# Performance work log

Hardware: AMD Instinct MI355X
Metric: run time of the kernel (lower is better)

## Reference

```python
import jax, jax.numpy as jnp
import numpy as np

N, E, R, D = 100000, 1600000, 8, 128

def setup_inputs() -> dict:
    key = jax.random.key(0)
    ks = jax.random.split(key, 8)
    x = jax.random.normal(ks[0], (N, D), dtype=jnp.float32)
    src = jax.random.randint(ks[1], (E,), 0, N, dtype=jnp.int32)
    dst = jax.random.randint(ks[2], (E,), 0, N, dtype=jnp.int32)
    etype = jax.random.randint(ks[3], (E,), 0, R, dtype=jnp.int32)
    W_rel = jax.random.normal(ks[4], (R, D, D), dtype=jnp.float32) * 0.05
    loop_w = jax.random.normal(ks[5], (D, D), dtype=jnp.float32) * 0.05
    rel_bias = jnp.zeros((D,), dtype=jnp.float32)
    W1 = jax.random.normal(ks[6], (2 * D, 2 * D), dtype=jnp.float32) * 0.05
    b1 = jnp.zeros((2 * D,), dtype=jnp.float32)
    W2 = jax.random.normal(ks[7], (3 * D, D), dtype=jnp.float32) * 0.05
    b2 = jnp.zeros((D,), dtype=jnp.float32)
    return {"x": x, "src": src, "dst": dst, "etype": etype,
            "W_rel": W_rel, "loop_w": loop_w, "rel_bias": rel_bias,
            "W1": W1, "b1": b1, "W2": W2, "b2": b2}

def reference(x, src, dst, etype, W_rel, loop_w, rel_bias, W1, b1, W2, b2):
    # RelGraphConv (low_mem): aggregate source features per (relation, dst) node,
    # then one matmul per relation: msg[i] = sum_r (sum_{e: etype=r, dst=i} x[src_e]) @ W_r
    seg = etype.astype(jnp.int32) * N + dst.astype(jnp.int32)  # combined (rel, dst) id
    agg = jax.ops.segment_sum(x[src], seg, num_segments=R * N)  # [R*N, D]
    agg = agg.reshape(R, N, D)
    msg = jnp.einsum('rnd,rdo->no', agg, W_rel)  # per-relation transform + sum over relations
    msg = msg + x @ loop_w + rel_bias            # DGL default self_loop + bias
    # concat-MLP update (activation = tanh)
    mid = jnp.tanh(jnp.concatenate([x, msg], axis=1) @ W1 + b1)  # [N, 2D]
    out = jnp.concatenate([x, mid], axis=1) @ W2 + b2            # [N, D]
    return out
```

## Files before the change

### kernel.cpp

```cpp
#include <hip/hip_runtime.h>

#define NN 100000
#define DD 128
#define RR 8
#define NSEG (RR*NN)
#define NB1 782
#define ECAP 2048

typedef unsigned short u16;
typedef __bf16 bf16x8 __attribute__((ext_vector_type(8)));
typedef float f32x4 __attribute__((ext_vector_type(4)));
typedef u16 ushort4e __attribute__((ext_vector_type(4)));
typedef unsigned int uint4e __attribute__((ext_vector_type(4)));

__device__ __forceinline__ u16 f2bf(float f){
    union { float f; unsigned u; } v; v.f = f;
    unsigned r = v.u + 0x7fffu + ((v.u >> 16) & 1u);
    return (u16)(r >> 16);
}
__device__ __forceinline__ float bf2f(u16 h){
    union { unsigned u; float f; } v; v.u = ((unsigned)h) << 16; return v.f;
}
__device__ __forceinline__ float ftanh(float x){
    float e = __expf(2.0f * x);
    return 1.0f - 2.0f / (e + 1.0f);
}
__device__ __forceinline__ bf16x8 ldv(const u16* p){
    return *reinterpret_cast<const bf16x8*>(p);
}
__device__ __forceinline__ void gload_lds16(const void* g, void* l){
    __builtin_amdgcn_global_load_lds(
        (const __attribute__((address_space(1))) void*)g,
        (__attribute__((address_space(3))) void*)l, 16, 0, 0);
}

__global__ void k_prep1(const float* __restrict__ x, u16* __restrict__ xb,
                        const float* __restrict__ Wrel, const float* __restrict__ loopw,
                        const float* __restrict__ W1, const float* __restrict__ W2,
                        u16* __restrict__ WT, u16* __restrict__ W1t, u16* __restrict__ W2t,
                        const int* __restrict__ et, const int* __restrict__ dst,
                        int* __restrict__ cnt, int* __restrict__ seg, int E){
    const int bid = blockIdx.x;
    if (bid < 12500){
        int i = (bid * 256 + threadIdx.x) * 4;
        float4 v = *reinterpret_cast<const float4*>(x + i);
        ushort4 o = make_ushort4(f2bf(v.x), f2bf(v.y), f2bf(v.z), f2bf(v.w));
        *reinterpret_cast<ushort4*>(xb + i) = o;
    } else if (bid < 13524){
        int tid = (bid - 12500) * 256 + threadIdx.x;
        if (tid < 131072) {
            int r = tid >> 14, rem = tid & 16383, d = rem >> 7, o = rem & 127;
            WT[(r * 128 + o) * 128 + d] = f2bf(Wrel[tid]);
        } else if (tid < 147456) {
            int i = tid - 131072, d = i >> 7, o = i & 127;
            WT[(8 * 128 + o) * 128 + d] = f2bf(loopw[i]);
        } else if (tid < 212992) {
            int i = tid - 147456, k = i >> 8, n2 = i & 255;
            W1t[n2 * 256 + k] = f2bf(W1[i]);
        } else {
            int i = tid - 212992, k = i >> 7, n2 = i & 127;
            W2t[n2 * 384 + k] = f2bf(W2[i]);
        }
    } else {
        int e = (bid - 13524) * 256 + threadIdx.x;
        if (e < E){
            int s = et[e] * NN + dst[e];
            seg[e] = s;
            atomicAdd(&cnt[s], 1);
        }
    }
}

__global__ void k_scan1(const int* __restrict__ cnt, int* __restrict__ Off, int* __restrict__ bsum){
    __shared__ int lds[256];
    int t = threadIdx.x;
    int i0 = blockIdx.x * 1024 + t * 4;
    int c0 = (i0 + 0 < NSEG) ? cnt[i0 + 0] : 0;
    int c1 = (i0 + 1 < NSEG) ? cnt[i0 + 1] : 0;
    int c2 = (i0 + 2 < NSEG) ? cnt[i0 + 2] : 0;
    int c3 = (i0 + 3 < NSEG) ? cnt[i0 + 3] : 0;
    int s = c0 + c1 + c2 + c3;
    lds[t] = s; __syncthreads();
    for (int off = 1; off < 256; off <<= 1){
        int v = (t >= off) ? lds[t - off] : 0;
        __syncthreads();
        lds[t] += v;
        __syncthreads();
    }
    int excl = lds[t] - s;
    if (i0 + 0 < NSEG) Off[i0 + 0] = excl; excl += c0;
    if (i0 + 1 < NSEG) Off[i0 + 1] = excl; excl += c1;
    if (i0 + 2 < NSEG) Off[i0 + 2] = excl; excl += c2;
    if (i0 + 3 < NSEG) Off[i0 + 3] = excl;
    if (t == 255) bsum[blockIdx.x] = s + lds[t] - s;
}

__global__ void k_scan3b(int* __restrict__ Off, const int* __restrict__ bsum,
                         int* __restrict__ cursor, int E){
    __shared__ int lds[256];
    const int bid = blockIdx.x;
    const int t = threadIdx.x;
    int s = 0;
    for (int j = t; j < bid; j += 256) s += bsum[j];
    lds[t] = s; __syncthreads();
    #pragma unroll
    for (int off = 128; off > 0; off >>= 1){
        if (t < off) lds[t] += lds[t + off];
        __syncthreads();
    }
    const int base = lds[0];
    int i0 = bid * 1024 + t * 4;
    #pragma unroll
    for (int j = 0; j < 4; ++j){
        int i = i0 + j;
        if (i < NSEG){ int v = Off[i] + base; Off[i] = v; cursor[i] = v; }
    }
    if (bid == 0 && t == 0) Off[NSEG] = E;
}

__global__ void k_scatter(const int* __restrict__ seg, const int* __restrict__ src,
                          int* __restrict__ cursor, int* __restrict__ esrc, int E){
    int e = blockIdx.x * 256 + threadIdx.x;
    if (e < E){
        int pos = atomicAdd(&cursor[seg[e]], 1);
        esrc[pos] = src[e];
    }
}

__global__ __launch_bounds__(256) void k_agg(
    const u16* __restrict__ xb, const int* __restrict__ Off,
    const int* __restrict__ esrc, u16* __restrict__ agg)
{
    __shared__ int offs[33];
    __shared__ int eidx[ECAP];
    const int tid = threadIdx.x;
    const int s0 = blockIdx.x * 32;
    if (tid < 33) offs[tid] = Off[s0 + tid];
    __syncthreads();
    const int base = offs[0];
    const int tot = offs[32] - base;
    const bool inlds = (tot <= ECAP);
    if (inlds){
        for (int i = tid; i < tot; i += 256) eidx[i] = esrc[base + i];
    }
    __syncthreads();

    const int hw = tid >> 5;
    const int lid = tid & 31;
    const int c = lid * 4;

    #pragma unroll
    for (int j = 0; j < 4; ++j){
        const int sj = hw * 4 + j;
        const int lo = offs[sj] - base;
        const int hi = offs[sj + 1] - base;
        float a0 = 0.f, a1 = 0.f, a2 = 0.f, a3 = 0.f;
        int e = lo;
        if (inlds){
            for (; e + 4 <= hi; e += 4){
                int i0 = eidx[e], i1 = eidx[e+1], i2 = eidx[e+2], i3 = eidx[e+3];
                ushort4 v0 = *reinterpret_cast<const ushort4*>(xb + (size_t)i0 * DD + c);
                ushort4 v1 = *reinterpret_cast<const ushort4*>(xb + (size_t)i1 * DD + c);
                ushort4 v2 = *reinterpret_cast<const ushort4*>(xb + (size_t)i2 * DD + c);
                ushort4 v3 = *reinterpret_cast<const ushort4*>(xb + (size_t)i3 * DD + c);
                a0 += bf2f(v0.x) + bf2f(v1.x) + bf2f(v2.x) + bf2f(v3.x);
                a1 += bf2f(v0.y) + bf2f(v1.y) + bf2f(v2.y) + bf2f(v3.y);
                a2 += bf2f(v0.z) + bf2f(v1.z) + bf2f(v2.z) + bf2f(v3.z);
                a3 += bf2f(v0.w) + bf2f(v1.w) + bf2f(v2.w) + bf2f(v3.w);
            }
            for (; e < hi; ++e){
                int i = eidx[e];
                ushort4 v = *reinterpret_cast<const ushort4*>(xb + (size_t)i * DD + c);
                a0 += bf2f(v.x); a1 += bf2f(v.y); a2 += bf2f(v.z); a3 += bf2f(v.w);
            }
        } else {
            for (; e < hi; ++e){
                int i = esrc[base + e];
                ushort4 v = *reinterpret_cast<const ushort4*>(xb + (size_t)i * DD + c);
                a0 += bf2f(v.x); a1 += bf2f(v.y); a2 += bf2f(v.z); a3 += bf2f(v.w);
            }
        }
        ushort4e o;
        o.x = f2bf(a0); o.y = f2bf(a1); o.z = f2bf(a2); o.w = f2bf(a3);
        __builtin_nontemporal_store(o,
            reinterpret_cast<ushort4e*>(agg + (size_t)(s0 + sj) * DD + c));
    }
}

__global__ __launch_bounds__(512) void k_fused(
    const u16* __restrict__ xb, const u16* __restrict__ agg,
    const u16* __restrict__ WT, const u16* __restrict__ W1t, const u16* __restrict__ W2t,
    const float* __restrict__ relb, const float* __restrict__ bb1, const float* __restrict__ bb2,
    float* __restrict__ out)
{
    __shared__ __align__(16) u16 smem[25088];
    u16 (*bufA)[128] = (u16(*)[128])(smem);
    u16 (*bufB)[128] = (u16(*)[128])(smem + 8192);
    u16 (*msgs)[136] = (u16(*)[136])(smem + 16384);
    u16 (*mids)[264] = (u16(*)[264])(smem + 8192);

    const int tid = threadIdx.x;
    const int w = tid >> 6;
    const int lane = tid & 63;
    const int l15 = lane & 15;
    const int l4 = lane >> 4;
    const int kof = l4 * 8;
    const int swz = (l15 & 7) << 3;
    const int b64 = blockIdx.x * 64;

    const int Wb0 = w * 1024 + (lane << 4);
    auto stage_dma = [&](u16* buf, const u16* grows){
        #pragma unroll
        for (int is = 0; is < 2; ++is){
            int W = Wb0 + is * 8192;
            int row = W >> 8;
            int srcrow = (b64 + row < NN) ? row : 0;
            int inrow = (W & 255) ^ ((row & 7) << 4);
            const char* src = (const char*)(grows + (size_t)srcrow * DD) + inrow;
            gload_lds16(src, (char*)buf + W);
        }
    };

    f32x4 acc[4];
    #pragma unroll
    for (int mi = 0; mi < 4; ++mi)
        #pragma unroll
        for (int q = 0; q < 4; ++q) acc[mi][q] = 0.f;

    stage_dma(&bufA[0][0], agg + (size_t)b64 * DD);
    __syncthreads();

    for (int r = 0; r <= 8; ++r){
        if (r < 7)       stage_dma((r & 1) ? &bufA[0][0] : &bufB[0][0],
                                   agg + ((size_t)(r + 1) * NN + b64) * DD);
        else if (r == 7) stage_dma(&bufA[0][0], xb + (size_t)b64 * DD);
        const u16 (*A)[128] = (r & 1) ? bufB : bufA;
        const u16* B = WT + r * (DD * DD);
        #pragma unroll
        for (int kc = 0; kc < 4; ++kc){
            int cA = (kc * 32 + kof) ^ swz;
            bf16x8 a0 = ldv(&A[l15][cA]);
            bf16x8 a1 = ldv(&A[16 + l15][cA]);
            bf16x8 a2 = ldv(&A[32 + l15][cA]);
            bf16x8 a3 = ldv(&A[48 + l15][cA]);
            bf16x8 wv = ldv(B + (w * 16 + l15) * DD + kc * 32 + kof);
            acc[0] = __builtin_amdgcn_mfma_f32_16x16x32_bf16(a0, wv, acc[0], 0, 0, 0);
            acc[1] = __builtin_amdgcn_mfma_f32_16x16x32_bf16(a1, wv, acc[1], 0, 0, 0);
            acc[2] = __builtin_amdgcn_mfma_f32_16x16x32_bf16(a2, wv, acc[2], 0, 0, 0);
            acc[3] = __builtin_amdgcn_mfma_f32_16x16x32_bf16(a3, wv, acc[3], 0, 0, 0);
        }
        __syncthreads();
    }

    {
        int col = w * 16 + l15;
        float bv = relb[col];
        #pragma unroll
        for (int mi = 0; mi < 4; ++mi)
            #pragma unroll
            for (int q = 0; q < 4; ++q)
                msgs[mi * 16 + l4 * 4 + q][col] = f2bf(acc[mi][q] + bv);
    }
    __syncthreads();

    f32x4 acc2[4][2];
    #pragma unroll
    for (int mi = 0; mi < 4; ++mi)
        #pragma unroll
        for (int nj = 0; nj < 2; ++nj)
            #pragma unroll
            for (int q = 0; q < 4; ++q) acc2[mi][nj][q] = 0.f;

    #pragma unroll
    for (int kc = 0; kc < 8; ++kc){
        bf16x8 a[4];
        #pragma unroll
        for (int mi = 0; mi < 4; ++mi)
            a[mi] = (kc < 4) ? ldv(&bufA[mi * 16 + l15][(kc * 32 + kof) ^ swz])
                             : ldv(&msgs[mi * 16 + l15][(kc - 4) * 32 + kof]);
        #pragma unroll
        for (int nj = 0; nj < 2; ++nj){
            int n2 = w * 32 + nj * 16 + l15;
            bf16x8 wv = ldv(W1t + n2 * 256 + kc * 32 + kof);
            #pragma unroll
            for (int mi = 0; mi < 4; ++mi)
                acc2[mi][nj] = __builtin_amdgcn_mfma_f32_16x16x32_bf16(a[mi], wv, acc2[mi][nj], 0, 0, 0);
        }
    }
    __syncthreads();
    #pragma unroll
    for (int nj = 0; nj < 2; ++nj){
        int col = w * 32 + nj * 16 + l15;
        float bv = bb1[col];
        #pragma unroll
        for (int mi = 0; mi < 4; ++mi)
            #pragma unroll
            for (int q = 0; q < 4; ++q)
                mids[mi * 16 + l4 * 4 + q][col] = f2bf(ftanh(acc2[mi][nj][q] + bv));
    }
    __syncthreads();

    f32x4 acc3[4];
    #pragma unroll
    for (int mi = 0; mi < 4; ++mi)
        #pragma unroll
        for (int q = 0; q < 4; ++q) acc3[mi][q] = 0.f;

    #pragma unroll
    for (int kc = 0; kc < 12; ++kc){
        bf16x8 a[4];
        #pragma unroll
        for (int mi = 0; mi < 4; ++mi)
            a[mi] = (kc < 4) ? ldv(&bufA[mi * 16 + l15][(kc * 32 + kof) ^ swz])
                             : ldv(&mids[mi * 16 + l15][(kc - 4) * 32 + kof]);
        bf16x8 wv = ldv(W2t + (w * 16 + l15) * 384 + kc * 32 + kof);
        #pragma unroll
        for (int mi = 0; mi < 4; ++mi)
            acc3[mi] = __builtin_amdgcn_mfma_f32_16x16x32_bf16(a[mi], wv, acc3[mi], 0, 0, 0);
    }

    {
        int col = w * 16 + l15;
        float bv = bb2[col];
        #pragma unroll
        for (int mi = 0; mi < 4; ++mi)
            #pragma unroll
            for (int q = 0; q < 4; ++q){
                int row = b64 + mi * 16 + l4 * 4 + q;
                if (row < NN)
                    __builtin_nontemporal_store(acc3[mi][q] + bv,
                        &out[(size_t)row * DD + col]);
            }
    }
}

extern "C" void kernel_launch(void* const* d_in, const int* in_sizes, int n_in,
                              void* d_out, int out_size, void* d_ws, size_t ws_size,
                              hipStream_t stream){
    const float* x    = (const float*)d_in[0];
    const int*   src  = (const int*)d_in[1];
    const int*   dst  = (const int*)d_in[2];
    const int*   et   = (const int*)d_in[3];
    const float* Wrel = (const float*)d_in[4];
    const float* loopw= (const float*)d_in[5];
    const float* relb = (const float*)d_in[6];
    const float* W1   = (const float*)d_in[7];
    const float* b1   = (const float*)d_in[8];
    const float* W2   = (const float*)d_in[9];
    const float* b2   = (const float*)d_in[10];
    const int E = in_sizes[1];
    float* out = (float*)d_out;

    char* ws = (char*)d_ws;
    u16* xb   = (u16*)(ws);
    u16* WT   = (u16*)(ws + 25600000);
    u16* W1t  = (u16*)(ws + 25894912);
    u16* W2t  = (u16*)(ws + 26025984);
    int* cnt  = (int*)(ws + 26124288);
    int* Off  = (int*)(ws + 29324288);
    int* bsum = (int*)(ws + 32524544);
    int* esrc = (int*)(ws + 32528640);
    u16* agg  = (u16*)(ws + 38928640);
    int* seg  = (int*)(ws + 38928640);
    if (ws_size < 243728640UL) return;

    const int gprep = 13524 + (E + 255) / 256;
    hipMemsetAsync(cnt, 0, NSEG * sizeof(int), stream);
    k_prep1<<<gprep, 256, 0, stream>>>(x, xb, Wrel, loopw, W1, W2, WT, W1t, W2t,
                                       et, dst, cnt, seg, E);
    k_scan1<<<NB1, 256, 0, stream>>>(cnt, Off, bsum);
    k_scan3b<<<NB1, 256, 0, stream>>>(Off, bsum, cnt, E);
    k_scatter<<<(E + 255) / 256, 256, 0, stream>>>(seg, src, cnt, esrc, E);
    k_agg<<<NSEG / 32, 256, 0, stream>>>(xb, Off, esrc, agg);
    k_fused<<<(NN + 63) / 64, 512, 0, stream>>>(xb, agg, WT, W1t, W2t, relb, b1, b2, out);
}
```

Baseline: 437.0 us.

## Deepen fused-kernel LDS prefetch to four stages with explicit vmcnt waits

```diff
diff --git a/kernel.cpp b/kernel.cpp
--- a/kernel.cpp
+++ b/kernel.cpp
@@ -92,7 +92,7 @@
     if (i0 + 1 < NSEG) Off[i0 + 1] = excl; excl += c1;
     if (i0 + 2 < NSEG) Off[i0 + 2] = excl; excl += c2;
     if (i0 + 3 < NSEG) Off[i0 + 3] = excl;
-    if (t == 255) bsum[blockIdx.x] = s + lds[t] - s;
+    if (t == 255) bsum[blockIdx.x] = lds[255];
 }
 
 __global__ void k_scan3b(int* __restrict__ Off, const int* __restrict__ bsum,
@@ -193,11 +193,10 @@
     const float* __restrict__ relb, const float* __restrict__ bb1, const float* __restrict__ bb2,
     float* __restrict__ out)
 {
-    __shared__ __align__(16) u16 smem[25088];
-    u16 (*bufA)[128] = (u16(*)[128])(smem);
-    u16 (*bufB)[128] = (u16(*)[128])(smem + 8192);
-    u16 (*msgs)[136] = (u16(*)[136])(smem + 16384);
-    u16 (*mids)[264] = (u16(*)[264])(smem + 8192);
+    __shared__ __align__(16) u16 smem[32768];
+    u16* xt   = smem;
+    u16* msgs = smem + 8192;
+    u16* mids = smem + 16384;
 
     const int tid = threadIdx.x;
     const int w = tid >> 6;
@@ -227,29 +226,44 @@
         #pragma unroll
         for (int q = 0; q < 4; ++q) acc[mi][q] = 0.f;
 
-    stage_dma(&bufA[0][0], agg + (size_t)b64 * DD);
-    __syncthreads();
+    #pragma unroll
+    for (int t = 0; t < 4; ++t)
+        stage_dma(smem + t * 8192, agg + ((size_t)t * NN + b64) * DD);
 
     for (int r = 0; r <= 8; ++r){
-        if (r < 7)       stage_dma((r & 1) ? &bufA[0][0] : &bufB[0][0],
-                                   agg + ((size_t)(r + 1) * NN + b64) * DD);
-        else if (r == 7) stage_dma(&bufA[0][0], xb + (size_t)b64 * DD);
-        const u16 (*A)[128] = (r & 1) ? bufB : bufA;
+        __builtin_amdgcn_sched_barrier(0);
+        if (r <= 5)      asm volatile("s_waitcnt vmcnt(6)" ::: "memory");
+        else if (r == 6) asm volatile("s_waitcnt vmcnt(4)" ::: "memory");
+        else if (r == 7) asm volatile("s_waitcnt vmcnt(2)" ::: "memory");
+        else             asm volatile("s_waitcnt vmcnt(0)" ::: "memory");
+        __builtin_amdgcn_sched_barrier(0);
+        __builtin_amdgcn_s_barrier();
+        __builtin_amdgcn_sched_barrier(0);
+
+        const u16* A = smem + (r & 3) * 8192;
         const u16* B = WT + r * (DD * DD);
         #pragma unroll
         for (int kc = 0; kc < 4; ++kc){
             int cA = (kc * 32 + kof) ^ swz;
-            bf16x8 a0 = ldv(&A[l15][cA]);
-            bf16x8 a1 = ldv(&A[16 + l15][cA]);
-            bf16x8 a2 = ldv(&A[32 + l15][cA]);
-            bf16x8 a3 = ldv(&A[48 + l15][cA]);
+            bf16x8 a0 = ldv(A + (l15) * 128 + cA);
+            bf16x8 a1 = ldv(A + (16 + l15) * 128 + cA);
+            bf16x8 a2 = ldv(A + (32 + l15) * 128 + cA);
+            bf16x8 a3 = ldv(A + (48 + l15) * 128 + cA);
             bf16x8 wv = ldv(B + (w * 16 + l15) * DD + kc * 32 + kof);
             acc[0] = __builtin_amdgcn_mfma_f32_16x16x32_bf16(a0, wv, acc[0], 0, 0, 0);
             acc[1] = __builtin_amdgcn_mfma_f32_16x16x32_bf16(a1, wv, acc[1], 0, 0, 0);
             acc[2] = __builtin_amdgcn_mfma_f32_16x16x32_bf16(a2, wv, acc[2], 0, 0, 0);
             acc[3] = __builtin_amdgcn_mfma_f32_16x16x32_bf16(a3, wv, acc[3], 0, 0, 0);
         }
-        __syncthreads();
+
+        asm volatile("s_waitcnt lgkmcnt(0)" ::: "memory");
+        __builtin_amdgcn_sched_barrier(0);
+        __builtin_amdgcn_s_barrier();
+        __builtin_amdgcn_sched_barrier(0);
+
+        if (r <= 3)      stage_dma(smem + (r & 3) * 8192,
+                                   agg + ((size_t)(r + 4) * NN + b64) * DD);
+        else if (r == 4) stage_dma(smem + 0 * 8192, xb + (size_t)b64 * DD);
     }
 
     {
@@ -258,8 +272,10 @@
         #pragma unroll
         for (int mi = 0; mi < 4; ++mi)
             #pragma unroll
-            for (int q = 0; q < 4; ++q)
-                msgs[mi * 16 + l4 * 4 + q][col] = f2bf(acc[mi][q] + bv);
+            for (int q = 0; q < 4; ++q){
+                int row = mi * 16 + l4 * 4 + q;
+                msgs[row * 128 + (col ^ ((row & 7) << 3))] = f2bf(acc[mi][q] + bv);
+            }
     }
     __syncthreads();
 
@@ -275,9 +291,11 @@
     for (int kc = 0; kc < 8; ++kc){
         bf16x8 a[4];
         #pragma unroll
-        for (int mi = 0; mi < 4; ++mi)
-            a[mi] = (kc < 4) ? ldv(&bufA[mi * 16 + l15][(kc * 32 + kof) ^ swz])
-                             : ldv(&msgs[mi * 16 + l15][(kc - 4) * 32 + kof]);
+        for (int mi = 0; mi < 4; ++mi){
+            int cA = ((kc & 3) * 32 + kof) ^ swz;
+            a[mi] = (kc < 4) ? ldv(xt + (mi * 16 + l15) * 128 + cA)
+                             : ldv(msgs + (mi * 16 + l15) * 128 + cA);
+        }
         #pragma unroll
         for (int nj = 0; nj < 2; ++nj){
             int n2 = w * 32 + nj * 16 + l15;
@@ -287,7 +305,6 @@
                 acc2[mi][nj] = __builtin_amdgcn_mfma_f32_16x16x32_bf16(a[mi], wv, acc2[mi][nj], 0, 0, 0);
         }
     }
-    __syncthreads();
     #pragma unroll
     for (int nj = 0; nj < 2; ++nj){
         int col = w * 32 + nj * 16 + l15;
@@ -295,8 +312,10 @@
         #pragma unroll
         for (int mi = 0; mi < 4; ++mi)
             #pragma unroll
-            for (int q = 0; q < 4; ++q)
-                mids[mi * 16 + l4 * 4 + q][col] = f2bf(ftanh(acc2[mi][nj][q] + bv));
+            for (int q = 0; q < 4; ++q){
+                int row = mi * 16 + l4 * 4 + q;
+                mids[row * 256 + (col ^ ((row & 7) << 3))] = f2bf(ftanh(acc2[mi][nj][q] + bv));
+            }
     }
     __syncthreads();
 
@@ -310,9 +329,15 @@
     for (int kc = 0; kc < 12; ++kc){
         bf16x8 a[4];
         #pragma unroll
-        for (int mi = 0; mi < 4; ++mi)
-            a[mi] = (kc < 4) ? ldv(&bufA[mi * 16 + l15][(kc * 32 + kof) ^ swz])
-                             : ldv(&mids[mi * 16 + l15][(kc - 4) * 32 + kof]);
+        for (int mi = 0; mi < 4; ++mi){
+            if (kc < 4){
+                int cA = (kc * 32 + kof) ^ swz;
+                a[mi] = ldv(xt + (mi * 16 + l15) * 128 + cA);
+            } else {
+                int cA = (((kc - 4) * 32) + kof) ^ swz;
+                a[mi] = ldv(mids + (mi * 16 + l15) * 256 + cA);
+            }
+        }
         bf16x8 wv = ldv(W2t + (w * 16 + l15) * 384 + kc * 32 + kof);
         #pragma unroll
         for (int mi = 0; mi < 4; ++mi)
```

Measured after the change: 443.7 us. No clear change (+1.5%).
